# Optimization experiments

Measured on AMD Instinct MI355X. Metric: run time of the kernel, lower is better.

## Reference

```python
import jax, jax.numpy as jnp
from jax import lax
import numpy as np

N_QUBITS = 8
Q_DEPTH = 10
DIM = 256  # 2**8

# basis-state bit table; wire 0 = most-significant bit (PennyLane convention)
_bits = ((np.arange(DIM)[:, None] >> (N_QUBITS - 1 - np.arange(N_QUBITS))) & 1)
# phase layer: S on even wires (phase i), T on odd wires (phase e^{i pi/4})
_ph = np.where(np.arange(N_QUBITS) % 2 == 0, 1j, np.exp(1j * np.pi / 4))
_diag = np.prod(np.power(_ph[None, :], _bits), axis=1)
# entangling_layer_3 CZ pattern
_cz = np.ones(DIM)
for i, j in [(0, 1), (2, 3), (4, 5), (6, 7), (1, 2), (3, 4), (5, 6)]:
    _cz = _cz * ((-1.0) ** (_bits[:, i] * _bits[:, j]))
DIAG = jnp.asarray((_diag * _cz).astype(np.complex64))  # phase+CZ layer fused diagonal
ZSIGNS = jnp.asarray((1 - 2 * _bits).astype(np.float32))  # [256, 8] PauliZ eigenvalues
H_GATE = jnp.asarray((np.array([[1.0, 1.0], [1.0, -1.0]]) / np.sqrt(2.0)).astype(np.complex64))
X_GATE = jnp.asarray(np.array([[0.0, 1.0], [1.0, 0.0]]).astype(np.complex64))
EYE2 = jnp.eye(2, dtype=jnp.complex64)
BN_EPS = 1e-5


def apply_1q(state, U, w):
    """Apply 2x2 gate U on wire w; state: [B, 2,2,...,2]."""
    state = jnp.moveaxis(state, w + 1, -1)
    state = jnp.matmul(state, U.T)
    return jnp.moveaxis(state, -1, w + 1)


def quantum_net(features, q_params):
    """Batched statevector sim of quantum_net_3. features [B,256], q_params [80] -> [B,8]."""
    f = features / jnp.linalg.norm(features, axis=1, keepdims=True)
    state = f.astype(jnp.complex64).reshape((-1,) + (2,) * N_QUBITS)
    for w in range(N_QUBITS):
        state = apply_1q(state, H_GATE, w)
    qw = q_params.reshape(Q_DEPTH, N_QUBITS)
    for layer in range(Q_DEPTH):
        for w in range(N_QUBITS):
            t = qw[layer, w]
            c = jnp.cos(t / 2).astype(jnp.complex64)
            s = jnp.sin(t / 2).astype(jnp.complex64)
            U = c * EYE2 + (-1j) * s * X_GATE  # RX(t)
            state = apply_1q(state, U, w)
        flat = state.reshape(-1, DIM) * DIAG  # phase layer + CZ entangling (diagonal)
        state = flat.reshape((-1,) + (2,) * N_QUBITS)
    sv = state.reshape(-1, DIM)
    probs = sv.real ** 2 + sv.imag ** 2
    return probs @ ZSIGNS  # [B, 8] expval(PauliZ_i)


def conv2d(x, w, b):
    y = lax.conv_general_dilated(x, w, (1, 1), 'SAME', dimension_numbers=('NCHW', 'OIHW', 'NCHW'))
    return y + b[None, :, None, None]


def bn(x, gamma, beta, mean, var):  # eval-mode BatchNorm2d
    inv = gamma / jnp.sqrt(var + BN_EPS)
    return x * inv[None, :, None, None] + (beta - mean * inv)[None, :, None, None]


def maxpool2(x):
    return lax.reduce_window(x, -jnp.inf, lax.max, (1, 1, 2, 2), (1, 1, 2, 2), 'VALID')


def setup_inputs() -> dict:
    key = jax.random.key(0)
    ks = jax.random.split(key, 16)
    B = 1024
    return {
        'x': jax.random.normal(ks[0], (B, 1, 28, 28), dtype=jnp.float32),
        'conv1_w': 0.1 * jax.random.normal(ks[1], (32, 1, 3, 3), dtype=jnp.float32),
        'conv1_b': jnp.zeros((32,), jnp.float32),
        'bn1_gamma': jnp.ones((32,), jnp.float32),
        'bn1_beta': jnp.zeros((32,), jnp.float32),
        'bn1_mean': jnp.zeros((32,), jnp.float32),
        'bn1_var': jnp.ones((32,), jnp.float32),
        'conv2_w': 0.05 * jax.random.normal(ks[2], (64, 32, 3, 3), dtype=jnp.float32),
        'conv2_b': jnp.zeros((64,), jnp.float32),
        'bn2_gamma': jnp.ones((64,), jnp.float32),
        'bn2_beta': jnp.zeros((64,), jnp.float32),
        'bn2_mean': jnp.zeros((64,), jnp.float32),
        'bn2_var': jnp.ones((64,), jnp.float32),
        'fc_w': 0.01 * jax.random.normal(ks[3], (256, 64 * 7 * 7), dtype=jnp.float32),
        'fc_b': jnp.zeros((256,), jnp.float32),
        'q_params': 0.1 * jax.random.normal(ks[4], (Q_DEPTH * N_QUBITS,), dtype=jnp.float32),
        'p1_w': 0.01 * jax.random.normal(ks[5], (128, 8), dtype=jnp.float32),
        'p1_b': jnp.zeros((128,), jnp.float32),
        'p2_w': 0.01 * jax.random.normal(ks[6], (64, 128), dtype=jnp.float32),
        'p2_b': jnp.zeros((64,), jnp.float32),
        'p3_w': 0.01 * jax.random.normal(ks[7], (10, 64), dtype=jnp.float32),
        'p3_b': jnp.zeros((10,), jnp.float32),
    }


def reference(x, conv1_w, conv1_b, bn1_gamma, bn1_beta, bn1_mean, bn1_var,
              conv2_w, conv2_b, bn2_gamma, bn2_beta, bn2_mean, bn2_var,
              fc_w, fc_b, q_params, p1_w, p1_b, p2_w, p2_b, p3_w, p3_b):
    h = maxpool2(jax.nn.relu(bn(conv2d(x, conv1_w, conv1_b), bn1_gamma, bn1_beta, bn1_mean, bn1_var)))
    h = maxpool2(jax.nn.relu(bn(conv2d(h, conv2_w, conv2_b), bn2_gamma, bn2_beta, bn2_mean, bn2_var)))
    h = h.reshape(h.shape[0], -1)  # [B, 64*7*7]
    feats = jnp.tanh(h @ fc_w.T + fc_b)  # [B, 256]
    q = quantum_net(feats, q_params)  # [B, 8]
    z = jax.nn.relu(q @ p1_w.T + p1_b)  # dropout = identity (eval)
    z = jax.nn.relu(z @ p2_w.T + p2_b)
    return z @ p3_w.T + p3_b
```

## Files before the change

### kernel.cpp

```cpp
#include <hip/hip_runtime.h>
#include <math.h>


#define B_SZ 1024

#define OFF_FCWP   0
#define OFF_W2F    802816
#define OFF_W1T    821248
#define OFF_SC1    821536
#define OFF_SH1    821568
#define OFF_SC2    821600
#define OFF_SH2    821664
#define OFF_H1     821728
#define OFF_P2WT   4500000
#define OFF_H2P    7244256

#define KSPLIT_FC 14
#define KCHUNK_FC 224

typedef __attribute__((ext_vector_type(8))) short s16x8;
typedef __attribute__((ext_vector_type(4))) float f32x4;

__constant__ float C_COS8[8] = {1.f, 0.70710678f, 0.f, -0.70710678f, -1.f, -0.70710678f, 0.f, 0.70710678f};
__constant__ float C_SIN8[8] = {0.f, 0.70710678f, 1.f, 0.70710678f, 0.f, -0.70710678f, -1.f, -0.70710678f};

__device__ __forceinline__ unsigned short bf16_rne(float f) {
  unsigned u = __float_as_uint(f);
  unsigned r = u + 0x7FFFu + ((u >> 16) & 1u);
  return (unsigned short)(r >> 16);
}
__device__ __forceinline__ int div14(int m) {
  return __float2int_rz((float)m * 0.07142858f);
}
__device__ __forceinline__ int swz16(int e) {
  return e ^ (((e >> 6) & 3) << 3);
}

__global__ __launch_bounds__(256) void prep_kernel(
    const float* __restrict__ fc_w, const float* __restrict__ c2w, const float* __restrict__ c1w,
    const float* __restrict__ bn1g, const float* __restrict__ bn1b, const float* __restrict__ bn1m,
    const float* __restrict__ bn1v, const float* __restrict__ c1b,
    const float* __restrict__ bn2g, const float* __restrict__ bn2b, const float* __restrict__ bn2m,
    const float* __restrict__ bn2v, const float* __restrict__ c2b,
    const float* __restrict__ p2w,
    float* __restrict__ ws) {
  int g = blockIdx.x * 256 + threadIdx.x;

  {
    int j = g & 7, lane = (g >> 3) & 63, nt = (g >> 9) & 15, kg = g >> 13;
    int n = nt * 16 + (lane & 15);
    int k = kg * 32 + ((lane >> 4) & 3) * 8 + j;
    float v = fc_w[n * 3136 + (k & 63) * 49 + (k >> 6)];
    unsigned short hi = bf16_rne(v);
    unsigned short lo = bf16_rne(v - __uint_as_float((unsigned)hi << 16));
    unsigned short* us = (unsigned short*)ws;
    int base = ((kg * 16 + nt) * 2) * 512 + lane * 8 + j;
    us[base] = hi;
    us[base + 512] = lo;
  }

  if (g < 36864) {
    int j = g & 7, L = (g >> 3) & 63, rest = g >> 9;
    int h = rest & 1; rest >>= 1;
    int t = rest % 9, w = rest / 9;
    int occ = w * 16 + (L & 15);
    int ic  = (L >> 4) * 8 + j;
    float v = c2w[occ * 288 + ic * 9 + t];
    unsigned short hi = bf16_rne(v);
    unsigned short res = hi;
    if (h) res = bf16_rne(v - __uint_as_float((unsigned)hi << 16));
    ((unsigned short*)(ws + OFF_W2F))[g] = res;
  }
  if (g < 8192) {
    ws[OFF_P2WT + g] = p2w[(g & 63) * 128 + (g >> 6)];
  }
  if (g < 288) {
    ws[OFF_W1T + g] = c1w[(g & 31) * 9 + (g >> 5)];
  }
  if (g < 32) {
    float inv = bn1g[g] / sqrtf(bn1v[g] + 1e-5f);
    ws[OFF_SC1 + g] = inv;
    ws[OFF_SH1 + g] = c1b[g] * inv + bn1b[g] - bn1m[g] * inv;
  }
  if (g < 64) {
    float inv = bn2g[g] / sqrtf(bn2v[g] + 1e-5f);
    ws[OFF_SC2 + g] = inv;
    ws[OFF_SH2 + g] = c2b[g] * inv + bn2b[g] - bn2m[g] * inv;
  }
}

__global__ __launch_bounds__(256, 3) void conv12_kernel(
    const float* __restrict__ x, const float* __restrict__ w1T,
    const float* __restrict__ sc1, const float* __restrict__ sh1,
    const float* __restrict__ w2f_f,
    const float* __restrict__ sc2, const float* __restrict__ sh2,
    unsigned short* __restrict__ h2hi, unsigned short* __restrict__ h2lo) {
  const int b = blockIdx.x, tid = threadIdx.x;
  const int lane = tid & 63, w = tid >> 6;

  __shared__ unsigned char lds_raw[50176];
  unsigned short* tile_hi = (unsigned short*)lds_raw;
  unsigned short* tile_lo = (unsigned short*)(lds_raw + 17408);
  float* xs  = (float*)(lds_raw + 34816);
  float* w1s = (float*)(lds_raw + 38656);
  float* sc1s = (float*)(lds_raw + 39808);
  float* sh1s = sc1s + 32;
  float* conv_out = (float*)lds_raw;

  {
    float4* z = (float4*)lds_raw;
    for (int i = tid; i < 2416; i += 256) z[i] = make_float4(0.f, 0.f, 0.f, 0.f);
  }
  __syncthreads();

  const float* xb = x + b * 784;
  for (int i = tid; i < 784; i += 256) {
    int y = i / 28, c = i - y * 28;
    xs[(y + 1) * 32 + (c + 1)] = xb[i];
  }
  for (int i = tid; i < 288; i += 256) w1s[i] = w1T[i];
  if (tid < 32) { sc1s[tid] = sc1[tid]; sh1s[tid] = sh1[tid]; }
  __syncthreads();

  for (int t = tid; t < 448; t += 256) {
    const int oc = t & 31, py = t >> 5;
    float wv[9];
#pragma unroll
    for (int k = 0; k < 9; ++k) wv[k] = w1s[k * 32 + oc];
    float acc0[28], acc1[28];
#pragma unroll
    for (int j = 0; j < 28; ++j) { acc0[j] = 0.f; acc1[j] = 0.f; }
#pragma unroll
    for (int r = 0; r < 4; ++r) {
      const int pr = 2 * py + r;
      float row[32];
#pragma unroll
      for (int q = 0; q < 8; ++q) {
        float4 v = *(const float4*)&xs[pr * 32 + 4 * q];
        row[4 * q] = v.x; row[4 * q + 1] = v.y; row[4 * q + 2] = v.z; row[4 * q + 3] = v.w;
      }
      if (r <= 2) {
#pragma unroll
        for (int kx = 0; kx < 3; ++kx) {
          const float w1v = wv[r * 3 + kx];
#pragma unroll
          for (int xx = 0; xx < 28; ++xx) acc0[xx] = fmaf(row[xx + kx], w1v, acc0[xx]);
        }
      }
      if (r >= 1) {
#pragma unroll
        for (int kx = 0; kx < 3; ++kx) {
          const float w1v = wv[(r - 1) * 3 + kx];
#pragma unroll
          for (int xx = 0; xx < 28; ++xx) acc1[xx] = fmaf(row[xx + kx], w1v, acc1[xx]);
        }
      }
    }
    const float sc = sc1s[oc], sh = sh1s[oc];
#pragma unroll
    for (int px = 0; px < 14; ++px) {
      float v0 = fmaxf(fmaf(acc0[2 * px], sc, sh), 0.f);
      float v1 = fmaxf(fmaf(acc0[2 * px + 1], sc, sh), 0.f);
      float v2 = fmaxf(fmaf(acc1[2 * px], sc, sh), 0.f);
      float v3 = fmaxf(fmaf(acc1[2 * px + 1], sc, sh), 0.f);
      float vm = fmaxf(fmaxf(v0, v1), fmaxf(v2, v3));
      unsigned short hv = bf16_rne(vm);
      unsigned short lv = bf16_rne(vm - __uint_as_float((unsigned)hv << 16));
      const int e = swz16(((py + 1) * 16 + (px + 1)) * 32 + oc);
      tile_hi[e] = hv;
      tile_lo[e] = lv;
    }
  }
  __syncthreads();

  const unsigned short* w2f = (const unsigned short*)w2f_f;
  s16x8 bf[9][2];
#pragma unroll
  for (int t = 0; t < 9; ++t)
#pragma unroll
    for (int h = 0; h < 2; ++h)
      bf[t][h] = *(const s16x8*)&w2f[(((w * 9 + t) * 2 + h) << 9) + lane * 8];

  f32x4 acc[13];
#pragma unroll
  for (int i = 0; i < 13; ++i) acc[i] = (f32x4){0.f, 0.f, 0.f, 0.f};

  const int kg8 = (lane >> 4) * 8;
#pragma unroll
  for (int mt = 0; mt < 13; ++mt) {
    const int m = mt * 16 + (lane & 15);
    const int y = div14(m), xx = m - y * 14;
    const int base = (y * 16 + xx) * 32 + kg8;
#pragma unroll
    for (int dy = 0; dy < 3; ++dy) {
#pragma unroll
      for (int dx = 0; dx < 3; ++dx) {
        const int off = swz16(base + (dy * 16 + dx) * 32);
        s16x8 ah = *(s16x8*)&tile_hi[off];
        s16x8 al = *(s16x8*)&tile_lo[off];
        const int t = dy * 3 + dx;
        acc[mt] = __builtin_amdgcn_mfma_f32_16x16x32_bf16(ah, bf[t][0], acc[mt], 0, 0, 0);
        acc[mt] = __builtin_amdgcn_mfma_f32_16x16x32_bf16(ah, bf[t][1], acc[mt], 0, 0, 0);
        acc[mt] = __builtin_amdgcn_mfma_f32_16x16x32_bf16(al, bf[t][0], acc[mt], 0, 0, 0);
      }
    }
  }
  __syncthreads();

  const int oc = w * 16 + (lane & 15);
  const float sc = sc2[oc], sh = sh2[oc];
  float* cw = conv_out + w * 3136;
#pragma unroll
  for (int mt = 0; mt < 13; ++mt) {
#pragma unroll
    for (int r = 0; r < 4; ++r) {
      const int m = mt * 16 + (lane >> 4) * 4 + r;
      if (m < 196) cw[m * 16 + (lane & 15)] = fmaxf(fmaf(acc[mt][r], sc, sh), 0.f);
    }
  }
  __syncthreads();

#pragma unroll
  for (int i = 0; i < 13; ++i) {
    const int ps = i * 4 + (lane >> 4);
    if (ps < 49) {
      const int py = (ps * 37) >> 8, px = ps - py * 7;
      const int m00 = py * 28 + px * 2;
      const int c0 = m00 * 16 + (lane & 15);
      float v0 = cw[c0], v1 = cw[c0 + 16], v2 = cw[c0 + 224], v3 = cw[c0 + 240];
      float vm = fmaxf(fmaxf(v0, v1), fmaxf(v2, v3));
      unsigned short hv = bf16_rne(vm);
      const int idx = b * 3136 + ps * 64 + oc;
      h2hi[idx] = hv;
      h2lo[idx] = bf16_rne(vm - __uint_as_float((unsigned)hv << 16));
    }
  }
}

__global__ __launch_bounds__(256) void fc_mfma_kernel(
    const unsigned short* __restrict__ h2hi, const unsigned short* __restrict__ h2lo,
    const unsigned short* __restrict__ Bfrag, float* __restrict__ Part) {
  __shared__ unsigned short Bs[4096];
  const int tid = threadIdx.x;
  const int lane = tid & 63, w = tid >> 6;
  const int m0 = blockIdx.y * 64, nt0 = blockIdx.x * 4, z = blockIdx.z;
  const int kz = z * KCHUNK_FC;

  const int mrow = m0 + w * 16 + (lane & 15);
  const int kg8 = (lane >> 4) * 8;
  const unsigned short* arow_hi = h2hi + mrow * 3136;
  const unsigned short* arow_lo = h2lo + mrow * 3136;

  f32x4 acc[4];
#pragma unroll
  for (int i = 0; i < 4; ++i) acc[i] = (f32x4){0.f, 0.f, 0.f, 0.f};

  s16x8 ah = *(const s16x8*)(arow_hi + kz + kg8);
  s16x8 al = *(const s16x8*)(arow_lo + kz + kg8);

  for (int c = 0; c < 7; ++c) {
    const int kg = (kz >> 5) + c;
    {
      const uint4* src = (const uint4*)(Bfrag + (size_t)(kg * 16 + nt0) * 1024);
      uint4* dst = (uint4*)Bs;
      dst[tid] = src[tid];
      dst[tid + 256] = src[tid + 256];
    }
    s16x8 ah2, al2;
    if (c < 6) {
      const int k1 = kz + (c + 1) * 32;
      ah2 = *(const s16x8*)(arow_hi + k1 + kg8);
      al2 = *(const s16x8*)(arow_lo + k1 + kg8);
    }
    __syncthreads();

#pragma unroll
    for (int nf = 0; nf < 4; ++nf) {
      s16x8 bh = *(s16x8*)&Bs[(nf * 2 + 0) * 512 + lane * 8];
      s16x8 bl = *(s16x8*)&Bs[(nf * 2 + 1) * 512 + lane * 8];
      acc[nf] = __builtin_amdgcn_mfma_f32_16x16x32_bf16(ah, bh, acc[nf], 0, 0, 0);
      acc[nf] = __builtin_amdgcn_mfma_f32_16x16x32_bf16(ah, bl, acc[nf], 0, 0, 0);
      acc[nf] = __builtin_amdgcn_mfma_f32_16x16x32_bf16(al, bh, acc[nf], 0, 0, 0);
    }
    __syncthreads();
    if (c < 6) { ah = ah2; al = al2; }
  }

  float* dst = Part + (size_t)z * 262144;
  const int mbase = m0 + w * 16 + (lane >> 4) * 4;
  const int nbase = nt0 * 16 + (lane & 15);
#pragma unroll
  for (int nf = 0; nf < 4; ++nf) {
#pragma unroll
    for (int r = 0; r < 4; ++r) {
      dst[(mbase + r) * 256 + nbase + nf * 16] = acc[nf][r];
    }
  }
}

__global__ __launch_bounds__(256) void quantum_kernel(
    const float* __restrict__ Part, const float* __restrict__ fc_b,
    const float* __restrict__ qp,
    const float* __restrict__ p1w, const float* __restrict__ p1b,
    const float* __restrict__ p2wT, const float* __restrict__ p2b,
    const float* __restrict__ p3w, const float* __restrict__ p3b,
    float* __restrict__ out) {
  const int tid = threadIdx.x;
  const int lane = tid & 63, wv = tid >> 6;
  const int b = blockIdx.x * 4 + wv;
  __shared__ float csl[160];
  __shared__ float z1buf[4][128];
  __shared__ float z2buf[4][64];

  if (tid < 80) {
    float t = 0.5f * qp[tid];
    csl[2 * tid] = cosf(t);
    csl[2 * tid + 1] = sinf(t);
  }
  __syncthreads();

  float f[4];
#pragma unroll
  for (int r = 0; r < 4; ++r) {
    const int n = r * 64 + lane;
    float a = fc_b[n];
#pragma unroll
    for (int z = 0; z < KSPLIT_FC; ++z) a += Part[z * 262144 + b * 256 + n];
    f[r] = tanhf(a);
  }
  float ss = (f[0] * f[0] + f[1] * f[1]) + (f[2] * f[2] + f[3] * f[3]);
#pragma unroll
  for (int off = 32; off >= 1; off >>= 1) ss += __shfl_xor(ss, off);
  const float inv = 1.0f / sqrtf(ss);
  float re[4], im[4];
#pragma unroll
  for (int r = 0; r < 4; ++r) { re[r] = f[r] * inv; im[r] = 0.f; }

  float dre[4], dim_[4];
#pragma unroll
  for (int r = 0; r < 4; ++r) {
    const int i = r * 64 + lane;
    const int k8 = (2 * __popc(i & 0xAA) + __popc(i & 0x55)) & 7;
    float dr = C_COS8[k8], di = C_SIN8[k8];
    int par = ((i >> 7) & (i >> 6)) ^ ((i >> 5) & (i >> 4)) ^ ((i >> 3) & (i >> 2)) ^ ((i >> 1) & i)
            ^ ((i >> 6) & (i >> 5)) ^ ((i >> 4) & (i >> 3)) ^ ((i >> 2) & (i >> 1));
    if (par & 1) { dr = -dr; di = -di; }
    dre[r] = dr; dim_[r] = di;
  }

  const float RS = 0.70710678118654752f;

  {
    float nr[4], ni[4];
#pragma unroll
    for (int r = 0; r < 4; ++r) {
      const float sgn = (r & 2) ? -1.f : 1.f;
      nr[r] = fmaf(sgn, re[r], re[r ^ 2]) * RS;
      ni[r] = fmaf(sgn, im[r], im[r ^ 2]) * RS;
    }
#pragma unroll
    for (int r = 0; r < 4; ++r) { re[r] = nr[r]; im[r] = ni[r]; }
  }
  {
    float nr[4], ni[4];
#pragma unroll
    for (int r = 0; r < 4; ++r) {
      const float sgn = (r & 1) ? -1.f : 1.f;
      nr[r] = fmaf(sgn, re[r], re[r ^ 1]) * RS;
      ni[r] = fmaf(sgn, im[r], im[r ^ 1]) * RS;
    }
#pragma unroll
    for (int r = 0; r < 4; ++r) { re[r] = nr[r]; im[r] = ni[r]; }
  }
#pragma unroll
  for (int w = 2; w < 8; ++w) {
    const int m = 1 << (7 - w);
    const float sgn = (lane & m) ? -1.f : 1.f;
#pragma unroll
    for (int r = 0; r < 4; ++r) {
      float pre = __shfl_xor(re[r], m);
      float pim = __shfl_xor(im[r], m);
      re[r] = fmaf(sgn, re[r], pre) * RS;
      im[r] = fmaf(sgn, im[r], pim) * RS;
    }
  }

  for (int layer = 0; layer < 10; ++layer) {
    const float* cs = &csl[16 * layer];
    {
      const float c = cs[0], s = cs[1];
      float nr[4], ni[4];
#pragma unroll
      for (int r = 0; r < 4; ++r) {
        nr[r] = fmaf(s, im[r ^ 2], c * re[r]);
        ni[r] = fmaf(-s, re[r ^ 2], c * im[r]);
      }
#pragma unroll
      for (int r = 0; r < 4; ++r) { re[r] = nr[r]; im[r] = ni[r]; }
    }
    {
      const float c = cs[2], s = cs[3];
      float nr[4], ni[4];
#pragma unroll
      for (int r = 0; r < 4; ++r) {
        nr[r] = fmaf(s, im[r ^ 1], c * re[r]);
        ni[r] = fmaf(-s, re[r ^ 1], c * im[r]);
      }
#pragma unroll
      for (int r = 0; r < 4; ++r) { re[r] = nr[r]; im[r] = ni[r]; }
    }
#pragma unroll
    for (int w = 2; w < 8; ++w) {
      const int m = 1 << (7 - w);
      const float c = cs[2 * w], s = cs[2 * w + 1];
#pragma unroll
      for (int r = 0; r < 4; ++r) {
        float pre = __shfl_xor(re[r], m);
        float pim = __shfl_xor(im[r], m);
        float nre = fmaf(s, pim, c * re[r]);
        float nim = fmaf(-s, pre, c * im[r]);
        if (w == 7) {
          float tre = nre * dre[r] - nim * dim_[r];
          nim = fmaf(nre, dim_[r], nim * dre[r]);
          nre = tre;
        }
        re[r] = nre; im[r] = nim;
      }
    }
  }

  float prb[4];
#pragma unroll
  for (int r = 0; r < 4; ++r) prb[r] = re[r] * re[r] + im[r] * im[r];
  float qv[8];
#pragma unroll
  for (int w = 0; w < 8; ++w) {
    float v;
    if (w == 0)      v = (prb[0] + prb[1]) - (prb[2] + prb[3]);
    else if (w == 1) v = (prb[0] + prb[2]) - (prb[1] + prb[3]);
    else {
      const int m = 1 << (7 - w);
      float s4 = (prb[0] + prb[1]) + (prb[2] + prb[3]);
      v = (lane & m) ? -s4 : s4;
    }
#pragma unroll
    for (int off = 32; off >= 1; off >>= 1) v += __shfl_xor(v, off);
    qv[w] = v;
  }

  {
    float a = p1b[lane], a2 = p1b[lane + 64];
#pragma unroll
    for (int k = 0; k < 8; ++k) {
      a  = fmaf(qv[k], p1w[lane * 8 + k], a);
      a2 = fmaf(qv[k], p1w[(lane + 64) * 8 + k], a2);
    }
    z1buf[wv][lane]      = fmaxf(a, 0.f);
    z1buf[wv][lane + 64] = fmaxf(a2, 0.f);
  }
  float acc2 = p2b[lane];
#pragma unroll 16
  for (int k = 0; k < 128; ++k)
    acc2 = fmaf(z1buf[wv][k], p2wT[k * 64 + lane], acc2);
  z2buf[wv][lane] = fmaxf(acc2, 0.f);

  if (lane < 10) {
    float a3 = p3b[lane];
#pragma unroll 16
    for (int k = 0; k < 64; ++k) a3 = fmaf(z2buf[wv][k], p3w[lane * 64 + k], a3);
    out[b * 10 + lane] = a3;
  }
}

extern "C" void kernel_launch(void* const* d_in, const int* in_sizes, int n_in,
                              void* d_out, int out_size, void* d_ws, size_t ws_size,
                              hipStream_t stream) {
  (void)in_sizes; (void)n_in; (void)out_size; (void)ws_size;
  const float* x    = (const float*)d_in[0];
  const float* c1w  = (const float*)d_in[1];
  const float* c1b  = (const float*)d_in[2];
  const float* bn1g = (const float*)d_in[3];
  const float* bn1b = (const float*)d_in[4];
  const float* bn1m = (const float*)d_in[5];
  const float* bn1v = (const float*)d_in[6];
  const float* c2w  = (const float*)d_in[7];
  const float* c2b  = (const float*)d_in[8];
  const float* bn2g = (const float*)d_in[9];
  const float* bn2b = (const float*)d_in[10];
  const float* bn2m = (const float*)d_in[11];
  const float* bn2v = (const float*)d_in[12];
  const float* fc_w = (const float*)d_in[13];
  const float* fc_b = (const float*)d_in[14];
  const float* qp   = (const float*)d_in[15];
  const float* p1w  = (const float*)d_in[16];
  const float* p1b  = (const float*)d_in[17];
  const float* p2w  = (const float*)d_in[18];
  const float* p2b  = (const float*)d_in[19];
  const float* p3w  = (const float*)d_in[20];
  const float* p3b  = (const float*)d_in[21];
  float* ws = (float*)d_ws;
  float* outp = (float*)d_out;

  unsigned short* h2hi = (unsigned short*)(ws + OFF_H2P);
  unsigned short* h2lo = h2hi + 3211264;
  const unsigned short* bfrag = (const unsigned short*)ws;

  prep_kernel<<<3136, 256, 0, stream>>>(fc_w, c2w, c1w,
                                        bn1g, bn1b, bn1m, bn1v, c1b,
                                        bn2g, bn2b, bn2m, bn2v, c2b, p2w, ws);
  conv12_kernel<<<B_SZ, 256, 0, stream>>>(x, ws + OFF_W1T, ws + OFF_SC1, ws + OFF_SH1,
                                          ws + OFF_W2F, ws + OFF_SC2, ws + OFF_SH2,
                                          h2hi, h2lo);
  fc_mfma_kernel<<<dim3(4, 16, KSPLIT_FC), 256, 0, stream>>>(h2hi, h2lo, bfrag, ws + OFF_H1);
  quantum_kernel<<<256, 256, 0, stream>>>(ws + OFF_H1, fc_b, qp, p1w, p1b,
                                          ws + OFF_P2WT, p2b, p3w, p3b, outp);
}
```

Before: 166.4 us.

## Split conv12 per-image work across two blocks with halo rows and smaller LDS

```diff
diff --git a/kernel.cpp b/kernel.cpp
--- a/kernel.cpp
+++ b/kernel.cpp
@@ -89,27 +89,28 @@
   }
 }
 
-__global__ __launch_bounds__(256, 3) void conv12_kernel(
+__global__ __launch_bounds__(256, 4) void conv12_kernel(
     const float* __restrict__ x, const float* __restrict__ w1T,
     const float* __restrict__ sc1, const float* __restrict__ sh1,
     const float* __restrict__ w2f_f,
     const float* __restrict__ sc2, const float* __restrict__ sh2,
     unsigned short* __restrict__ h2hi, unsigned short* __restrict__ h2lo) {
-  const int b = blockIdx.x, tid = threadIdx.x;
+  const int b = blockIdx.x >> 1, hh = blockIdx.x & 1;
+  const int tid = threadIdx.x;
   const int lane = tid & 63, w = tid >> 6;
 
-  __shared__ unsigned char lds_raw[50176];
+  __shared__ unsigned char lds_raw[25728];
   unsigned short* tile_hi = (unsigned short*)lds_raw;
-  unsigned short* tile_lo = (unsigned short*)(lds_raw + 17408);
-  float* xs  = (float*)(lds_raw + 34816);
-  float* w1s = (float*)(lds_raw + 38656);
-  float* sc1s = (float*)(lds_raw + 39808);
-  float* sh1s = sc1s + 32;
+  unsigned short* tile_lo = (unsigned short*)(lds_raw + 10240);
+  float* xs  = (float*)(lds_raw + 20480);
+  float* w1s = (float*)(lds_raw + 24320);
+  float* sc1s = (float*)(lds_raw + 25472);
+  float* sh1s = (float*)(lds_raw + 25600);
   float* conv_out = (float*)lds_raw;
 
   {
     float4* z = (float4*)lds_raw;
-    for (int i = tid; i < 2416; i += 256) z[i] = make_float4(0.f, 0.f, 0.f, 0.f);
+    for (int i = tid; i < 1520; i += 256) z[i] = make_float4(0.f, 0.f, 0.f, 0.f);
   }
   __syncthreads();
 
@@ -122,8 +123,9 @@
   if (tid < 32) { sc1s[tid] = sc1[tid]; sh1s[tid] = sh1[tid]; }
   __syncthreads();
 
-  for (int t = tid; t < 448; t += 256) {
-    const int oc = t & 31, py = t >> 5;
+  const int nitems = (9 - 2 * hh) * 32;
+  for (int t = tid; t < nitems; t += 256) {
+    const int oc = t & 31, py = (t >> 5) + 7 * hh;
     float wv[9];
 #pragma unroll
     for (int k = 0; k < 9; ++k) wv[k] = w1s[k * 32 + oc];
@@ -157,6 +159,7 @@
       }
     }
     const float sc = sc1s[oc], sh = sh1s[oc];
+    const int tw = py + 1 - 8 * hh;
 #pragma unroll
     for (int px = 0; px < 14; ++px) {
       float v0 = fmaxf(fmaf(acc0[2 * px], sc, sh), 0.f);
@@ -166,7 +169,7 @@
       float vm = fmaxf(fmaxf(v0, v1), fmaxf(v2, v3));
       unsigned short hv = bf16_rne(vm);
       unsigned short lv = bf16_rne(vm - __uint_as_float((unsigned)hv << 16));
-      const int e = swz16(((py + 1) * 16 + (px + 1)) * 32 + oc);
+      const int e = swz16((tw * 16 + (px + 1)) * 32 + oc);
       tile_hi[e] = hv;
       tile_lo[e] = lv;
     }
@@ -181,16 +184,18 @@
     for (int h = 0; h < 2; ++h)
       bf[t][h] = *(const s16x8*)&w2f[(((w * 9 + t) * 2 + h) << 9) + lane * 8];
 
-  f32x4 acc[13];
-#pragma unroll
-  for (int i = 0; i < 13; ++i) acc[i] = (f32x4){0.f, 0.f, 0.f, 0.f};
-
+  f32x4 acc[7];
+#pragma unroll
+  for (int i = 0; i < 7; ++i) acc[i] = (f32x4){0.f, 0.f, 0.f, 0.f};
+
+  const int MT0 = 7 * hh;
+  const int NMT = 7 - hh;
   const int kg8 = (lane >> 4) * 8;
-#pragma unroll
-  for (int mt = 0; mt < 13; ++mt) {
+  for (int i = 0; i < NMT; ++i) {
+    const int mt = MT0 + i;
     const int m = mt * 16 + (lane & 15);
     const int y = div14(m), xx = m - y * 14;
-    const int base = (y * 16 + xx) * 32 + kg8;
+    const int base = ((y - 8 * hh) * 16 + xx) * 32 + kg8;
 #pragma unroll
     for (int dy = 0; dy < 3; ++dy) {
 #pragma unroll
@@ -199,9 +204,9 @@
         s16x8 ah = *(s16x8*)&tile_hi[off];
         s16x8 al = *(s16x8*)&tile_lo[off];
         const int t = dy * 3 + dx;
-        acc[mt] = __builtin_amdgcn_mfma_f32_16x16x32_bf16(ah, bf[t][0], acc[mt], 0, 0, 0);
-        acc[mt] = __builtin_amdgcn_mfma_f32_16x16x32_bf16(ah, bf[t][1], acc[mt], 0, 0, 0);
-        acc[mt] = __builtin_amdgcn_mfma_f32_16x16x32_bf16(al, bf[t][0], acc[mt], 0, 0, 0);
+        acc[i] = __builtin_amdgcn_mfma_f32_16x16x32_bf16(ah, bf[t][0], acc[i], 0, 0, 0);
+        acc[i] = __builtin_amdgcn_mfma_f32_16x16x32_bf16(ah, bf[t][1], acc[i], 0, 0, 0);
+        acc[i] = __builtin_amdgcn_mfma_f32_16x16x32_bf16(al, bf[t][0], acc[i], 0, 0, 0);
       }
     }
   }
@@ -209,31 +214,44 @@
 
   const int oc = w * 16 + (lane & 15);
   const float sc = sc2[oc], sh = sh2[oc];
-  float* cw = conv_out + w * 3136;
-#pragma unroll
-  for (int mt = 0; mt < 13; ++mt) {
-#pragma unroll
-    for (int r = 0; r < 4; ++r) {
-      const int m = mt * 16 + (lane >> 4) * 4 + r;
-      if (m < 196) cw[m * 16 + (lane & 15)] = fmaxf(fmaf(acc[mt][r], sc, sh), 0.f);
-    }
-  }
-  __syncthreads();
-
-#pragma unroll
-  for (int i = 0; i < 13; ++i) {
-    const int ps = i * 4 + (lane >> 4);
-    if (ps < 49) {
-      const int py = (ps * 37) >> 8, px = ps - py * 7;
-      const int m00 = py * 28 + px * 2;
-      const int c0 = m00 * 16 + (lane & 15);
-      float v0 = cw[c0], v1 = cw[c0 + 16], v2 = cw[c0 + 224], v3 = cw[c0 + 240];
-      float vm = fmaxf(fmaxf(v0, v1), fmaxf(v2, v3));
-      unsigned short hv = bf16_rne(vm);
-      const int idx = b * 3136 + ps * 64 + oc;
-      h2hi[idx] = hv;
-      h2lo[idx] = bf16_rne(vm - __uint_as_float((unsigned)hv << 16));
-    }
+  float* cw = conv_out + w * 1024;
+  const int quad = lane >> 4, oc16 = lane & 15;
+
+#pragma unroll
+  for (int ch = 0; ch < 2; ++ch) {
+    const int wm = hh ? (ch ? 160 : 112) : (ch ? 48 : 0);
+    const int mtLo = hh ? (ch ? 10 : 7) : (ch ? 3 : 0);
+    const int mtHi = hh ? (ch ? 12 : 10) : (ch ? 6 : 3);
+    const int pb = hh ? (ch ? 42 : 28) : (ch ? 14 : 0);
+    const int pcnt = (hh && ch) ? 7 : 14;
+
+    for (int mt = mtLo; mt <= mtHi; ++mt) {
+      const int i = mt - MT0;
+#pragma unroll
+      for (int r = 0; r < 4; ++r) {
+        const int m = mt * 16 + quad * 4 + r;
+        if (m >= wm && m < wm + 64 && m < 196)
+          cw[(m - wm) * 16 + oc16] = fmaxf(fmaf(acc[i][r], sc, sh), 0.f);
+      }
+    }
+    __syncthreads();
+
+    for (int j = 0; j < 4; ++j) {
+      const int po = j * 4 + quad;
+      if (po < pcnt) {
+        const int ps = pb + po;
+        const int py = (ps * 37) >> 8, px = ps - py * 7;
+        const int m00 = py * 28 + px * 2;
+        const int c0 = (m00 - wm) * 16 + oc16;
+        float v0 = cw[c0], v1 = cw[c0 + 16], v2 = cw[c0 + 224], v3 = cw[c0 + 240];
+        float vm = fmaxf(fmaxf(v0, v1), fmaxf(v2, v3));
+        unsigned short hv = bf16_rne(vm);
+        const int idx = b * 3136 + ps * 64 + oc;
+        h2hi[idx] = hv;
+        h2lo[idx] = bf16_rne(vm - __uint_as_float((unsigned)hv << 16));
+      }
+    }
+    __syncthreads();
   }
 }
 
@@ -508,9 +526,9 @@
   prep_kernel<<<3136, 256, 0, stream>>>(fc_w, c2w, c1w,
                                         bn1g, bn1b, bn1m, bn1v, c1b,
                                         bn2g, bn2b, bn2m, bn2v, c2b, p2w, ws);
-  conv12_kernel<<<B_SZ, 256, 0, stream>>>(x, ws + OFF_W1T, ws + OFF_SC1, ws + OFF_SH1,
-                                          ws + OFF_W2F, ws + OFF_SC2, ws + OFF_SH2,
-                                          h2hi, h2lo);
+  conv12_kernel<<<2 * B_SZ, 256, 0, stream>>>(x, ws + OFF_W1T, ws + OFF_SC1, ws + OFF_SH1,
+                                              ws + OFF_W2F, ws + OFF_SC2, ws + OFF_SH2,
+                                              h2hi, h2lo);
   fc_mfma_kernel<<<dim3(4, 16, KSPLIT_FC), 256, 0, stream>>>(h2hi, h2lo, bfrag, ws + OFF_H1);
   quantum_kernel<<<256, 256, 0, stream>>>(ws + OFF_H1, fc_b, qp, p1w, p1b,
                                           ws + OFF_P2WT, p2b, p3w, p3b, outp);
```

Measured after the change: 174.6 us. +5.0%, slower.
